# Optimization experiments

Measured on AMD Instinct MI355X. Metric: run time of the kernel, lower is better.

Reference implementation:

```python
import jax, jax.numpy as jnp
import numpy as np

GRID_DIM = 7  # margin = 0, so each grid cell is a disjoint (H//g, W//g) tile


def setup_inputs() -> dict:
    key = jax.random.key(0)
    k1, k2 = jax.random.split(key)
    B, H, W, C = 8, 224, 224, 256
    NQ = 64
    images = jax.random.normal(k1, (B, H, W, C), dtype=jnp.float32)
    queries = jax.random.normal(k2, (NQ, C), dtype=jnp.float32)
    return {"images": images, "queries": queries}


def reference(images, queries):
    # images: [B, H, W, C]; queries: [NQ, C]
    B, H, W, C = images.shape
    g = GRID_DIM
    hs, ws = H // g, W // g  # tile size per grid cell (margin = 0)
    # Crop all g*g cells at once: [B, g, hs, g, ws, C] -> [B, g*g, L, C]
    # Cell index n = i*g + j (i over height, j over width) matches the
    # original positions ordering (pos[0] -> height, pos[1] -> width).
    regions = images.reshape(B, g, hs, g, ws, C)
    regions = regions.transpose(0, 1, 3, 2, 4, 5).reshape(B, g * g, hs * ws, C)
    # keras.layers.Attention default: unscaled dot-product + softmax.
    scores = jnp.einsum('qc,bnlc->bnql', queries, regions)  # [B, g*g, NQ, L]
    attn = jax.nn.softmax(scores, axis=-1)
    out = jnp.einsum('bnql,bnlc->bnqc', attn, regions)      # [B, g*g, NQ, C]
    return out
```

## Files before the change

### kernel.cpp

```cpp
#include <hip/hip_runtime.h>

typedef _Float16 half8 __attribute__((ext_vector_type(8)));
typedef _Float16 half4 __attribute__((ext_vector_type(4)));
typedef float f32x4  __attribute__((ext_vector_type(4)));

#define DEVI __device__ __forceinline__

constexpr int Bc = 8;
constexpr int Hc = 224;
constexpr int Wc = 224;
constexpr int Cc = 256;
constexpr int NQ = 64;
constexpr int TS = 32;
constexpr int Lc = TS * TS;
constexpr int KL = 64;
constexpr int NT = Lc / KL;

DEVI int subidx(int l, int c) {
  return ((((l >> 2) << 4) | (c >> 4)) << 6) | (((l & 3) << 4) | (c & 15));
}

DEVI uint ldsoff(const void* p) {
  return (uint)(uintptr_t)(const __attribute__((address_space(3))) char*)p;
}

union H2U { _Float16 h[2]; uint u; };

__global__ __launch_bounds__(256, 2) void attn_cells(
    const float* __restrict__ img,
    const float* __restrict__ qry,
    float* __restrict__ out)
{
  __shared__ _Float16 Rlds[2][KL * Cc];
  __shared__ _Float16 Plds[4][16 * KL];
  __shared__ float    Slds[NQ];
  __shared__ float    Llds[NQ];

  const int tid  = threadIdx.x;
  const int w    = tid >> 6;
  const int lane = tid & 63;
  const int lp   = lane & 15;
  const int gq   = lane >> 4;

  const int bn = blockIdx.x;
  const int b  = bn / 49;
  const int n  = bn % 49;
  const int i0 = n / 7, j0 = n % 7;

  const long cellbase = (((long)b * Hc + i0 * TS) * Wc + j0 * TS) * Cc;

  int goff[8], lds_off[8];
  #pragma unroll
  for (int s = 0; s < 8; ++s) {
    int G   = s * 256 + tid;
    int blk = G >> 3, sub = G & 7;
    int l   = ((blk >> 4) << 2) | ((sub >> 1) & 3);
    int c   = ((blk & 15) << 4) | ((sub & 1) << 3);
    int y   = l >> 5, x = l & 31;
    goff[s]    = (y * Wc + x) * Cc + c;
    lds_off[s] = G << 3;
  }

  half8 bq[8];
  {
    const int qrow = (w << 4) | lp;
    #pragma unroll
    for (int kc = 0; kc < 8; ++kc) {
      const float* qp = &qry[qrow * Cc + kc * 32 + gq * 8];
      f32x4 lo = *(const f32x4*)qp;
      f32x4 hi = *(const f32x4*)(qp + 4);
      half8 h;
      #pragma unroll
      for (int j = 0; j < 4; ++j) { h[j] = (_Float16)lo[j]; h[j + 4] = (_Float16)hi[j]; }
      bq[kc] = h;
    }
  }

  f32x4 acc[4][4];
  #pragma unroll
  for (int qb = 0; qb < 4; ++qb)
    #pragma unroll
    for (int cb = 0; cb < 4; ++cb) acc[qb][cb] = f32x4{0.f, 0.f, 0.f, 0.f};

  float mrun = -3.0e38f;
  float lsum = 0.0f;

  {
    const float* gb = img + cellbase;
    #pragma unroll
    for (int s = 0; s < 8; ++s) {
      f32x4 lo = *(const f32x4*)&gb[goff[s]];
      f32x4 hi = *(const f32x4*)&gb[goff[s] + 4];
      half8 h;
      #pragma unroll
      for (int j = 0; j < 4; ++j) { h[j] = (_Float16)lo[j]; h[j + 4] = (_Float16)hi[j]; }
      *(half8*)&Rlds[0][lds_off[s]] = h;
    }
  }
  __syncthreads();

  const uint trlane = (uint)(gq * 4096 + w * 512 +
                             ((((lp >> 2) << 4) | ((lp & 3) << 2)) << 1));

  for (int t = 0; t < NT; ++t) {
    const int pb = t & 1;
    const _Float16* Rbuf = &Rlds[pb][0];
    const uint trbase = ldsoff(Rbuf) + trlane;

    if (t + 1 < NT) {
      const float* gb = img + cellbase + (long)(t + 1) * (2 * Wc * Cc);
      _Float16* Rn = &Rlds[pb ^ 1][0];
      #pragma unroll
      for (int s = 0; s < 8; ++s) {
        f32x4 lo = *(const f32x4*)&gb[goff[s]];
        f32x4 hi = *(const f32x4*)&gb[goff[s] + 4];
        half8 h;
        #pragma unroll
        for (int j = 0; j < 4; ++j) { h[j] = (_Float16)lo[j]; h[j + 4] = (_Float16)hi[j]; }
        *(half8*)&Rn[lds_off[s]] = h;
      }
    }

    f32x4 sv[4];
    #pragma unroll
    for (int lb = 0; lb < 4; ++lb) sv[lb] = f32x4{0.f, 0.f, 0.f, 0.f};
    #pragma unroll
    for (int kc = 0; kc < 8; ++kc) {
      #pragma unroll
      for (int lb = 0; lb < 4; ++lb) {
        half8 a = *(const half8*)&Rbuf[subidx(lb * 16 + lp, kc * 32 + gq * 8)];
        sv[lb] = __builtin_amdgcn_mfma_f32_16x16x32_f16(a, bq[kc], sv[lb], 0, 0, 0);
      }
    }

    float cmax = sv[0][0];
    #pragma unroll
    for (int lb = 0; lb < 4; ++lb)
      #pragma unroll
      for (int r = 0; r < 4; ++r) cmax = fmaxf(cmax, sv[lb][r]);
    cmax = fmaxf(cmax, __shfl_xor(cmax, 16));
    cmax = fmaxf(cmax, __shfl_xor(cmax, 32));

    float mnew  = fmaxf(mrun, cmax);
    float scale = __expf(mrun - mnew);

    float ps = 0.0f;
    float pv[4][4];
    #pragma unroll
    for (int lb = 0; lb < 4; ++lb)
      #pragma unroll
      for (int r = 0; r < 4; ++r) {
        float p = __expf(sv[lb][r] - mnew);
        pv[lb][r] = p; ps += p;
      }
    ps += __shfl_xor(ps, 16);
    ps += __shfl_xor(ps, 32);
    lsum = lsum * scale + ps;
    mrun = mnew;

    {
      char* Pw = (char*)&Plds[w][0];
      #pragma unroll
      for (int lb = 0; lb < 4; ++lb) {
        H2U lo, hi;
        lo.h[0] = (_Float16)pv[lb][0]; lo.h[1] = (_Float16)pv[lb][1];
        hi.h[0] = (_Float16)pv[lb][2]; hi.h[1] = (_Float16)pv[lb][3];
        int base = lp * 128 + lb * 32 + gq * 8;
        int swz  = (lp & 7) << 4;
        *(uint*)(Pw + ((base ^ swz)))     = lo.u;
        *(uint*)(Pw + ((base ^ swz) + 4)) = hi.u;
      }
      if (lane < 16) Slds[w * 16 + lp] = scale;
    }

    __syncthreads();

    #pragma unroll
    for (int qb = 0; qb < 4; ++qb) {
      f32x4 sc = *(const f32x4*)&Slds[qb * 16 + gq * 4];
      #pragma unroll
      for (int cb = 0; cb < 4; ++cb) acc[qb][cb] *= sc;
    }

    #pragma unroll
    for (int kc = 0; kc < 2; ++kc) {
      half8 pa[4];
      #pragma unroll
      for (int qb = 0; qb < 4; ++qb) {
        const char* Pr = (const char*)&Plds[qb][0];
        int off = (lp * 128 + gq * 16 + kc * 64) ^ ((lp & 7) << 4);
        pa[qb] = *(const half8*)(Pr + off);
      }
      half4 tr[4][2];
      #pragma unroll
      for (int cb = 0; cb < 4; ++cb) {
        #pragma unroll
        for (int u = 0; u < 2; ++u) {
          asm volatile("ds_read_b64_tr_b16 %0, %1 offset:%2"
                       : "=v"(tr[cb][u])
                       : "v"(trbase), "i"(kc * 16384 + u * 2048 + cb * 128));
        }
      }
      asm volatile("s_waitcnt lgkmcnt(0)" ::: "memory");
      __builtin_amdgcn_sched_barrier(0);

      #pragma unroll
      for (int qb = 0; qb < 4; ++qb)
        #pragma unroll
        for (int cb = 0; cb < 4; ++cb) {
          half8 bv = __builtin_shufflevector(tr[cb][0], tr[cb][1], 0, 1, 2, 3, 4, 5, 6, 7);
          acc[qb][cb] = __builtin_amdgcn_mfma_f32_16x16x32_f16(pa[qb], bv, acc[qb][cb], 0, 0, 0);
        }
    }

    __syncthreads();
  }

  if (lane < 16) Llds[w * 16 + lp] = lsum;
  __syncthreads();

  float* ob = out + (long)bn * NQ * Cc;
  #pragma unroll
  for (int qb = 0; qb < 4; ++qb) {
    f32x4 lv = *(const f32x4*)&Llds[qb * 16 + gq * 4];
    #pragma unroll
    for (int r = 0; r < 4; ++r) {
      const float iv = 1.0f / lv[r];
      const int q = qb * 16 + gq * 4 + r;
      #pragma unroll
      for (int cb = 0; cb < 4; ++cb) {
        const int c = w * 64 + cb * 16 + lp;
        ob[q * Cc + c] = acc[qb][cb][r] * iv;
      }
    }
  }
}

extern "C" void kernel_launch(void* const* d_in, const int* in_sizes, int n_in,
                              void* d_out, int out_size, void* d_ws, size_t ws_size,
                              hipStream_t stream) {
  const float* img = (const float*)d_in[0];
  const float* qry = (const float*)d_in[1];
  float* outp      = (float*)d_out;
  dim3 grid(Bc * 49), block(256);
  attn_cells<<<grid, block, 0, stream>>>(img, qry, outp);
}
```

Before: 95.29 us.

## Defer prefetch LDS store after MFMA compute and use packed fp16 conversion

Next-tile global loads are now issued into 16 f32x4 staging registers at the start of each iteration. The fp16 convert and LDS write happen only after both MFMA phases, so global memory latency overlaps the score and PV compute instead of stalling before it. Conversions now use the packed cvt_pkrtz instruction, which rounds toward zero rather than to nearest and needs fewer instructions. The staging array adds 64 VGPRs per thread, which may cause spills or strain the 2-blocks-per-CU launch bound.

```diff
diff --git a/kernel.cpp b/kernel.cpp
--- a/kernel.cpp
+++ b/kernel.cpp
@@ -2,6 +2,7 @@
 
 typedef _Float16 half8 __attribute__((ext_vector_type(8)));
 typedef _Float16 half4 __attribute__((ext_vector_type(4)));
+typedef __fp16   fp16x2 __attribute__((ext_vector_type(2)));
 typedef float f32x4  __attribute__((ext_vector_type(4)));
 
 #define DEVI __device__ __forceinline__
@@ -24,7 +25,8 @@
   return (uint)(uintptr_t)(const __attribute__((address_space(3))) char*)p;
 }
 
-union H2U { _Float16 h[2]; uint u; };
+union PKU { fp16x2 h; uint u; };
+DEVI uint pkrtz(float a, float b) { PKU x; x.h = __builtin_amdgcn_cvt_pkrtz(a, b); return x.u; }
 
 __global__ __launch_bounds__(256, 2) void attn_cells(
     const float* __restrict__ img,
@@ -91,10 +93,10 @@
     for (int s = 0; s < 8; ++s) {
       f32x4 lo = *(const f32x4*)&gb[goff[s]];
       f32x4 hi = *(const f32x4*)&gb[goff[s] + 4];
-      half8 h;
-      #pragma unroll
-      for (int j = 0; j < 4; ++j) { h[j] = (_Float16)lo[j]; h[j + 4] = (_Float16)hi[j]; }
-      *(half8*)&Rlds[0][lds_off[s]] = h;
+      uint4 pk;
+      pk.x = pkrtz(lo[0], lo[1]); pk.y = pkrtz(lo[2], lo[3]);
+      pk.z = pkrtz(hi[0], hi[1]); pk.w = pkrtz(hi[2], hi[3]);
+      *(uint4*)&Rlds[0][lds_off[s]] = pk;
     }
   }
   __syncthreads();
@@ -107,17 +109,13 @@
     const _Float16* Rbuf = &Rlds[pb][0];
     const uint trbase = ldsoff(Rbuf) + trlane;
 
+    f32x4 stg[16];
     if (t + 1 < NT) {
       const float* gb = img + cellbase + (long)(t + 1) * (2 * Wc * Cc);
-      _Float16* Rn = &Rlds[pb ^ 1][0];
       #pragma unroll
       for (int s = 0; s < 8; ++s) {
-        f32x4 lo = *(const f32x4*)&gb[goff[s]];
-        f32x4 hi = *(const f32x4*)&gb[goff[s] + 4];
-        half8 h;
-        #pragma unroll
-        for (int j = 0; j < 4; ++j) { h[j] = (_Float16)lo[j]; h[j + 4] = (_Float16)hi[j]; }
-        *(half8*)&Rn[lds_off[s]] = h;
+        stg[2 * s]     = *(const f32x4*)&gb[goff[s]];
+        stg[2 * s + 1] = *(const f32x4*)&gb[goff[s] + 4];
       }
     }
 
@@ -162,13 +160,12 @@
       char* Pw = (char*)&Plds[w][0];
       #pragma unroll
       for (int lb = 0; lb < 4; ++lb) {
-        H2U lo, hi;
-        lo.h[0] = (_Float16)pv[lb][0]; lo.h[1] = (_Float16)pv[lb][1];
-        hi.h[0] = (_Float16)pv[lb][2]; hi.h[1] = (_Float16)pv[lb][3];
+        uint lo = pkrtz(pv[lb][0], pv[lb][1]);
+        uint hi = pkrtz(pv[lb][2], pv[lb][3]);
         int base = lp * 128 + lb * 32 + gq * 8;
         int swz  = (lp & 7) << 4;
-        *(uint*)(Pw + ((base ^ swz)))     = lo.u;
-        *(uint*)(Pw + ((base ^ swz) + 4)) = hi.u;
+        *(uint*)(Pw + ((base ^ swz)))     = lo;
+        *(uint*)(Pw + ((base ^ swz) + 4)) = hi;
       }
       if (lane < 16) Slds[w * 16 + lp] = scale;
     }
@@ -211,6 +208,19 @@
           half8 bv = __builtin_shufflevector(tr[cb][0], tr[cb][1], 0, 1, 2, 3, 4, 5, 6, 7);
           acc[qb][cb] = __builtin_amdgcn_mfma_f32_16x16x32_f16(pa[qb], bv, acc[qb][cb], 0, 0, 0);
         }
+    }
+
+    if (t + 1 < NT) {
+      _Float16* Rn = &Rlds[pb ^ 1][0];
+      #pragma unroll
+      for (int s = 0; s < 8; ++s) {
+        uint4 pk;
+        pk.x = pkrtz(stg[2 * s][0], stg[2 * s][1]);
+        pk.y = pkrtz(stg[2 * s][2], stg[2 * s][3]);
+        pk.z = pkrtz(stg[2 * s + 1][0], stg[2 * s + 1][1]);
+        pk.w = pkrtz(stg[2 * s + 1][2], stg[2 * s + 1][3]);
+        *(uint4*)&Rn[lds_off[s]] = pk;
+      }
     }
 
     __syncthreads();
```

Measured after the change: 96.97 us. No clear change (+1.8%).
